# Optimization experiments

Measured on AMD Instinct MI355X. Metric: run time of the kernel, lower is better.

## Reference

```python
import jax, jax.numpy as jnp
import numpy as np

B, N, C = 64, 256, 512
SHIFTS = (-1, 0, 1)
# torch.chunk(N, 3): ceil(256/3)=86 -> sizes [86, 86, 84]
CHUNK_SIZES = (86, 86, 84)
EPS = 1e-5


def _shift_pad(a, s):
    # shift along last axis (C) with zero padding, matching shift_with_padding
    if s == 0:
        return a
    if s > 0:
        return jnp.pad(a[..., :-s], ((0, 0), (0, 0), (s, 0)))
    s = -s
    return jnp.pad(a[..., s:], ((0, 0), (0, 0), (0, s)))


def setup_inputs() -> dict:
    key = jax.random.key(0)
    ks = jax.random.split(key, 16)
    w = lambda k, shape: (jax.random.normal(k, shape, jnp.float32) * 0.02)
    inp = {
        "x": jax.random.normal(ks[0], (B, N, C), jnp.float32),
        "ln_g": jnp.ones((C,), jnp.float32),
        "ln_b": jnp.zeros((C,), jnp.float32),
        "Ws": w(ks[1], (C, C)),
        "bs": jnp.zeros((C,), jnp.float32),
        "Wc": w(ks[2], (N, N, 3)),     # Conv1d weight [out=N, in=N, k=3]
        "bc": jnp.zeros((N,), jnp.float32),
        "We1": w(ks[3], (N, N // 8)),
        "be1": jnp.zeros((N // 8,), jnp.float32),
        "We2": w(ks[4], (N // 8, N)),
        "be2": jnp.zeros((N,), jnp.float32),
        "Wf1": w(ks[5], (C, 2 * C)),
        "bf1": jnp.zeros((2 * C,), jnp.float32),
        "Wf2": w(ks[6], (2 * C, C)),
        "bf2": jnp.zeros((C,), jnp.float32),
    }
    return inp


def reference(x, ln_g, ln_b, Ws, bs, Wc, bc, We1, be1, We2, be2, Wf1, bf1, Wf2, bf2):
    res = x
    # channel_mixer_S: LayerNorm over C, then Linear C->C + relu (dropout=0)
    mu = jnp.mean(x, axis=-1, keepdims=True)
    var = jnp.mean((x - mu) ** 2, axis=-1, keepdims=True)
    h = (x - mu) * jax.lax.rsqrt(var + EPS) * ln_g + ln_b
    h = jax.nn.relu(h @ Ws + bs)                      # [B, N, C]
    # channel_shift: chunk along N, shift each chunk along C with zero pad
    offs = np.cumsum((0,) + CHUNK_SIZES)
    chunks = [h[:, offs[i]:offs[i + 1], :] for i in range(3)]
    x_shift = jnp.concatenate([_shift_pad(c, s) for c, s in zip(chunks, SHIFTS)], axis=1)
    # channel_projection: Conv1d over C with N channels, k=3, pad=1
    x_shift = jax.lax.conv_general_dilated(
        x_shift, Wc, window_strides=(1,), padding=[(1, 1)],
        dimension_numbers=("NCH", "OIH", "NCH")) + bc[None, :, None]
    # SE gating
    se = jnp.mean(x_shift, axis=-1)                   # [B, N]
    ex = jax.nn.sigmoid(jax.nn.relu(se @ We1 + be1) @ We2 + be2)  # [B, N]
    z = x_shift * ex[:, :, None]
    # channel_mixer_F: C -> 2C (relu) -> C, residual
    z = jax.nn.relu(z @ Wf1 + bf1) @ Wf2 + bf2 + res
    return z
```

## Files before the change

kernel.cpp:

```cpp
#include <hip/hip_runtime.h>
#include <hip/hip_bf16.h>
#include <math.h>

#define BB 64
#define NN 256
#define CCH 512

typedef unsigned short u16;
typedef __attribute__((ext_vector_type(8))) short s16x8;
typedef __attribute__((ext_vector_type(4))) float f32x4;

#define AS1 __attribute__((address_space(1)))
#define AS3 __attribute__((address_space(3)))

static __device__ __forceinline__ u16 f2b(float f) {
    __hip_bfloat16 h = __float2bfloat16(f);
    union { __hip_bfloat16 h; u16 u; } x; x.h = h; return x.u;
}
static __device__ __forceinline__ void gll16(const void* g, void* l) {
    __builtin_amdgcn_global_load_lds((const AS1 unsigned int*)g,
                                     (AS3 unsigned int*)l, 16, 0, 0);
}
static __device__ __forceinline__ int shf(int ni) {
    return (ni < 86) ? -1 : (ni < 172 ? 0 : 1);
}

#define VM8  asm volatile("s_waitcnt vmcnt(8)" ::: "memory")
#define VM6  asm volatile("s_waitcnt vmcnt(6)" ::: "memory")
#define VM0  asm volatile("s_waitcnt vmcnt(0)" ::: "memory")
#define LGKM0 asm volatile("s_waitcnt lgkmcnt(0)" ::: "memory")
#define MEMB asm volatile("" ::: "memory")

static __device__ __forceinline__ void wtc_body(const float* __restrict__ W,
    u16* __restrict__ Wt, int K, int N, int bx, int by, float* t, bool perm)
{
    int n0 = bx * 32, k0 = by * 32;
    int tx = threadIdx.x & 31, ty = threadIdx.x >> 5;
    #pragma unroll
    for (int i = 0; i < 4; ++i)
        t[(ty + i * 8) * 33 + tx] = W[(size_t)(k0 + ty + i * 8) * N + n0 + tx];
    __syncthreads();
    int kl = k0 + tx;
    int kp = perm ? ((kl & ~63) | ((kl & 15) << 2) | ((kl >> 4) & 3)) : kl;
    #pragma unroll
    for (int i = 0; i < 4; ++i)
        Wt[(size_t)(n0 + ty + i * 8) * K + kp] = f2b(t[tx * 33 + ty + i * 8]);
}

__global__ __launch_bounds__(256) void prep_ln_kernel(
    const float* __restrict__ Ws,  u16* __restrict__ Wst,
    const float* __restrict__ Wf1, u16* __restrict__ Wf1t,
    const float* __restrict__ Wf2, u16* __restrict__ Wf2t,
    const float* __restrict__ Wc,  u16* __restrict__ Wc3,
    u16* __restrict__ Hts,
    const float* __restrict__ x, const float* __restrict__ g,
    const float* __restrict__ bta, u16* __restrict__ xnorm)
{
    __shared__ float t[32 * 33];
    int bid = blockIdx.x;
    if (bid < 256) {
        wtc_body(Ws, Wst, 512, 512, bid & 15, bid >> 4, t, false);
    } else if (bid < 768) {
        int idx = bid - 256;
        wtc_body(Wf1, Wf1t, 512, 1024, idx & 31, idx >> 5, t, true);
    } else if (bid < 1280) {
        int idx = bid - 768;
        wtc_body(Wf2, Wf2t, 1024, 512, idx & 15, idx >> 4, t, true);
    } else if (bid < 2048) {
        int idx = (bid - 1280) * 256 + threadIdx.x;
        int xloc = idx & 255;
        int o = (idx >> 8) & 255;
        int k = idx >> 16;
        int il = (xloc & ~63) | ((xloc & 63) >> 2) | ((xloc & 3) << 4);
        Wc3[idx] = f2b(Wc[((size_t)o * NN + il) * 3 + k]);
    } else if (bid < 2304) {
        int idx = (bid - 2048) * 256 + threadIdx.x;
        int b   = idx >> 10;
        int rem = idx & 1023;
        int rr  = rem >> 8;
        int r   = (rr & 1) + (rr >> 1) * 512;
        Hts[((size_t)b * 514 + r) * 256 + (rem & 255)] = 0;
    } else {
        const int l = threadIdx.x & 63;
        const int r = (bid - 2304) * 4 + (threadIdx.x >> 6);
        const float4* xr = (const float4*)(x + (size_t)r * CCH);
        float4 v1 = xr[l];
        float4 v2 = xr[l + 64];
        float s  = v1.x + v1.y + v1.z + v1.w + v2.x + v2.y + v2.z + v2.w;
        float ss = v1.x*v1.x + v1.y*v1.y + v1.z*v1.z + v1.w*v1.w
                 + v2.x*v2.x + v2.y*v2.y + v2.z*v2.z + v2.w*v2.w;
        #pragma unroll
        for (int o = 32; o > 0; o >>= 1) {
            s  += __shfl_xor(s, o);
            ss += __shfl_xor(ss, o);
        }
        float mu  = s * (1.0f / CCH);
        float var = ss * (1.0f / CCH) - mu * mu;
        float rs  = rsqrtf(var + 1e-5f);
        float4 g1 = ((const float4*)g)[l],   g2 = ((const float4*)g)[l + 64];
        float4 b1 = ((const float4*)bta)[l], b2 = ((const float4*)bta)[l + 64];
        ushort4 o1, o2;
        o1.x = f2b((v1.x - mu) * rs * g1.x + b1.x);
        o1.y = f2b((v1.y - mu) * rs * g1.y + b1.y);
        o1.z = f2b((v1.z - mu) * rs * g1.z + b1.z);
        o1.w = f2b((v1.w - mu) * rs * g1.w + b1.w);
        o2.x = f2b((v2.x - mu) * rs * g2.x + b2.x);
        o2.y = f2b((v2.y - mu) * rs * g2.y + b2.y);
        o2.z = f2b((v2.z - mu) * rs * g2.z + b2.z);
        o2.w = f2b((v2.w - mu) * rs * g2.w + b2.w);
        ushort4* orow = (ushort4*)(xnorm + (size_t)r * CCH);
        orow[l]      = o1;
        orow[l + 64] = o2;
    }
}

template<int MODE>
__global__ __launch_bounds__(512, 1) void gemm_pipe(
    const u16* __restrict__ A, const u16* __restrict__ Bt,
    const float* __restrict__ bias, const float* __restrict__ res,
    void* __restrict__ outv, u16* __restrict__ auxout,
    float* __restrict__ SEpart)
{
    constexpr int NK = (MODE == 2) ? 32 : (MODE == 3) ? 24 : 16;
    constexpr int SA = (MODE == 2) ? 1024 : 512;
    constexpr int SB = (MODE == 2) ? 1024 : 512;

    __shared__ u16 Asm[6 * 8192];
    __shared__ u16 Bsm[6 * 4096];

    const int tid = threadIdx.x;
    const int l   = tid & 63;
    const int w   = tid >> 6;
    const int nwg = gridDim.x;
    const int work = (blockIdx.x & 7) * (nwg >> 3) + (blockIdx.x >> 3);

    int row0, col0, bidx = 0;
    if (MODE == 0)      { row0 = (work >> 7) * 256; col0 = (work & 127) * 128; }
    else if (MODE == 2) { row0 = (work >> 2) * 256; col0 = (work & 3) * 128; }
    else                { row0 = 0; bidx = work >> 2; col0 = (work & 3) * 128; }

    const u16* Aab  = A + (size_t)row0 * SA;
    const u16* Bab  = Bt + (size_t)col0 * SB;
    const u16* HtsB = Bt + (size_t)bidx * 514 * 256;

    const int wm = (w >> 1) * 64;
    const int wn = (w & 1) * 64;
    const int fr = l & 15;
    const int q  = l >> 4;
    const int kofs = ((q ^ ((l >> 1) & 3)) * 8);

    const f32x4 zero = {0.0f, 0.0f, 0.0f, 0.0f};
    f32x4 acc[4][4];
    #pragma unroll
    for (int m = 0; m < 4; ++m)
        #pragma unroll
        for (int n = 0; n < 4; ++n) acc[m][n] = zero;

    const int kc0 = ((tid & 3) ^ ((tid >> 3) & 3)) * 8;
    const int srow = tid >> 2;

    auto stage = [&](int u, int slot) {
        u16* ald = Asm + slot * 8192 + w * 512;
        u16* bld = Bsm + slot * 4096 + w * 512;
        if (MODE == 3) {
            const int kseg = u >> 3, kb = (u & 7) * 32 + kc0;
            gll16(A + kseg * 65536 + srow * 256 + kb, ald);
            gll16(A + kseg * 65536 + (srow + 128) * 256 + kb, ald + 4096);
            gll16(HtsB + (size_t)(col0 + srow + kseg) * 256 + kb, bld);
        } else {
            const int kb = u * 32 + kc0;
            gll16(Aab + (size_t)srow * SA + kb, ald);
            gll16(Aab + (size_t)(srow + 128) * SA + kb, ald + 4096);
            gll16(Bab + (size_t)srow * SB + kb, bld);
        }
    };

    stage(0, 0); stage(1, 1); stage(2, 2); stage(3, 3);
    int sa = 0;
    constexpr int NV = NK / 2;
    for (int v = 0; v < NV; ++v) {
        if (v + 1 < NV) { VM6; } else { VM0; }
        __builtin_amdgcn_s_barrier();
        MEMB;
        const int sb = sa + 1;
        s16x8 b0[4], af0[4];
        #pragma unroll
        for (int n = 0; n < 4; ++n)
            b0[n] = *(const s16x8*)&Bsm[sa * 4096 + (wn + n * 16 + fr) * 32 + kofs];
        #pragma unroll
        for (int m = 0; m < 4; ++m)
            af0[m] = *(const s16x8*)&Asm[sa * 8192 + (wm + m * 16 + fr) * 32 + kofs];
        const int u2 = 2 * v + 4;
        if (u2 < NK) {
            int st = sa + 4; if (st >= 6) st -= 6;
            stage(u2, st);
            int st1 = st + 1; if (st1 >= 6) st1 -= 6;
            stage(u2 + 1, st1);
        }
        __builtin_amdgcn_s_setprio(1);
        #pragma unroll
        for (int m = 0; m < 4; ++m)
            #pragma unroll
            for (int n = 0; n < 4; ++n)
                acc[m][n] = __builtin_amdgcn_mfma_f32_16x16x32_bf16(af0[m], b0[n], acc[m][n], 0, 0, 0);
        __builtin_amdgcn_s_setprio(0);
        s16x8 b1[4], af1[4];
        #pragma unroll
        for (int n = 0; n < 4; ++n)
            b1[n] = *(const s16x8*)&Bsm[sb * 4096 + (wn + n * 16 + fr) * 32 + kofs];
        #pragma unroll
        for (int m = 0; m < 4; ++m)
            af1[m] = *(const s16x8*)&Asm[sb * 8192 + (wm + m * 16 + fr) * 32 + kofs];
        __builtin_amdgcn_s_setprio(1);
        #pragma unroll
        for (int m = 0; m < 4; ++m)
            #pragma unroll
            for (int n = 0; n < 4; ++n)
                acc[m][n] = __builtin_amdgcn_mfma_f32_16x16x32_bf16(af1[m], b1[n], acc[m][n], 0, 0, 0);
        __builtin_amdgcn_s_setprio(0);
        MEMB;
        sa += 2; if (sa >= 6) sa = 0;
    }

    if (MODE == 0) {
        const int gb = col0 + wn;
        const int b  = gb >> 8;
        const int gl = gb & 255;
        const int nib = gl + fr;
        u16* HtsW = auxout + (size_t)b * 514 * 256;
        const int px = gl + 4 * fr;
        const int s0 = shf(nib), s3 = shf(nib + 48);
        #pragma unroll
        for (int m = 0; m < 4; ++m) {
            #pragma unroll
            for (int j = 0; j < 4; ++j) {
                const int c = row0 + wm + m * 16 + q * 4 + j;
                const float bsv = bias[c];
                u16 vv[4];
                #pragma unroll
                for (int n = 0; n < 4; ++n)
                    vv[n] = f2b(fmaxf(acc[m][n][j] + bsv, 0.0f));
                if (s0 == s3) {
                    ushort4 v4 = {vv[0], vv[1], vv[2], vv[3]};
                    *(ushort4*)&HtsW[(size_t)(c + 1 + s0) * 256 + px] = v4;
                } else {
                    #pragma unroll
                    for (int n = 0; n < 4; ++n)
                        HtsW[(size_t)(c + 1 + shf(nib + n * 16)) * 256 + px + n] = vv[n];
                }
            }
        }
    } else if (MODE == 2) {
        #pragma unroll
        for (int m = 0; m < 4; ++m) {
            #pragma unroll
            for (int j = 0; j < 4; ++j) {
                const int row = row0 + wm + m * 16 + q * 4 + j;
                #pragma unroll
                for (int n = 0; n < 4; ++n) {
                    const int col = col0 + wn + n * 16 + fr;
                    ((float*)outv)[(size_t)row * 512 + col] =
                        acc[m][n][j] + bias[col] + res[(size_t)row * 512 + col];
                }
            }
        }
    } else {
        const int cb = col0 + wn;
        const int px = cb + 4 * fr;
        const int sslot = (col0 >> 7) * 2 + (wn >> 6);
        #pragma unroll
        for (int m = 0; m < 4; ++m) {
            #pragma unroll
            for (int j = 0; j < 4; ++j) {
                const int no = wm + m * 16 + q * 4 + j;
                const float bcv = bias[no];
                float p = 0.0f;
                u16 vv[4];
                #pragma unroll
                for (int n = 0; n < 4; ++n) {
                    float v = acc[m][n][j];
                    vv[n] = f2b(v + bcv);
                    p += v;
                }
                ushort4 v4 = {vv[0], vv[1], vv[2], vv[3]};
                *(ushort4*)&auxout[((size_t)bidx * NN + no) * CCH + px] = v4;
                p += __shfl_xor(p, 1);
                p += __shfl_xor(p, 2);
                p += __shfl_xor(p, 4);
                p += __shfl_xor(p, 8);
                if (fr == 0)
                    SEpart[sslot * 16384 + bidx * NN + no] = p;
            }
        }
    }
}

__global__ __launch_bounds__(512, 1) void gemm1_8ph(
    const u16* __restrict__ Yb, const u16* __restrict__ Wf1t,
    const float* __restrict__ bf1, u16* __restrict__ T,
    const float* __restrict__ SEpart, const float* __restrict__ bc,
    const float* __restrict__ We1, const float* __restrict__ be1,
    const float* __restrict__ We2, const float* __restrict__ be2)
{
    __shared__ u16 Ab[2][256 * 64];
    __shared__ u16 Bb[2][256 * 64];
    __shared__ float sse[256];
    __shared__ float e1f[32];
    __shared__ float exs[256];

    const int tid = threadIdx.x;
    const int l   = tid & 63;
    const int w   = tid >> 6;
    const int work = (blockIdx.x & 7) * 32 + (blockIdx.x >> 3);
    const int row0 = (work >> 2) * 256;
    const int col0 = (work & 3) * 256;

    const u16* Aab = Yb  + (size_t)row0 * 512;
    const u16* Bab = Wf1t + (size_t)col0 * 512;

    const int wm = (w >> 2) * 128;
    const int wn = (w & 3) * 64;
    const int fr = l & 15;
    const int q  = l >> 4;
    const int r7 = fr & 7;

    if (tid < 256) {
        int o = row0 + tid;
        float sum = 0.0f;
        #pragma unroll
        for (int i = 0; i < 8; ++i) sum += SEpart[i * 16384 + o];
        sse[tid] = sum * (1.0f / CCH) + bc[tid];
    }
    __syncthreads();
    if (tid < 32) {
        float a = be1[tid];
        #pragma unroll 8
        for (int i = 0; i < 256; ++i) a += sse[i] * We1[i * 32 + tid];
        e1f[tid] = fmaxf(a, 0.0f);
    }
    __syncthreads();
    if (tid < 256) {
        float a = be2[tid];
        #pragma unroll
        for (int j = 0; j < 32; ++j) a += e1f[j] * We2[j * 256 + tid];
        exs[tid] = 1.0f / (1.0f + expf(-a));
    }
    __syncthreads();

    const int strow = tid >> 3;
    const int sslot = tid & 7;
    const int gslot = sslot ^ (strow & 7);
    const size_t goff = (size_t)strow * 512 + gslot * 8;
    const int     loff = strow * 64 + sslot * 8;

    auto stageA = [&](int c, int kt, int j) {
        gll16(Aab + (size_t)(j * 64) * 512 + kt * 64 + goff,
              &Ab[c][j * 64 * 64 + loff]);
    };
    auto stageB = [&](int c, int kt, int j) {
        gll16(Bab + (size_t)(j * 64) * 512 + kt * 64 + goff,
              &Bb[c][j * 64 * 64 + loff]);
    };

    stageA(0, 0, 0); stageA(0, 0, 1); stageA(0, 0, 2); stageA(0, 0, 3);
    stageB(0, 0, 0); stageB(0, 0, 1); stageB(0, 0, 2); stageB(0, 0, 3);
    stageA(1, 1, 0); stageA(1, 1, 2);
    stageB(1, 1, 0); stageB(1, 1, 1); stageB(1, 1, 2); stageB(1, 1, 3);

    const f32x4 zero = {0.0f, 0.0f, 0.0f, 0.0f};
    f32x4 acc[8][4];
    #pragma unroll
    for (int m = 0; m < 8; ++m)
        #pragma unroll
        for (int n = 0; n < 4; ++n) acc[m][n] = zero;

    s16x8 afv[4][2], bfv[4][2];

#define LDA8(c, r, ks) (*(const s16x8*)&Ab[c][(r) * 64 + (((((ks) << 2) + q) ^ r7) << 3)])
#define LDB8(c, r, ks) (*(const s16x8*)&Bb[c][(r) * 64 + (((((ks) << 2) + q) ^ r7) << 3)])

    for (int t = 0; t < 8; ++t) {
        const int c = t & 1;
        if (t < 7) { stageA(c ^ 1, t + 1, 1); stageA(c ^ 1, t + 1, 3); VM8; }
        else       { VM0; }
        __builtin_amdgcn_s_barrier();
        MEMB;
        #pragma unroll
        for (int m = 0; m < 4; ++m) {
            afv[m][0] = LDA8(c, wm + m * 16 + fr, 0);
            afv[m][1] = LDA8(c, wm + m * 16 + fr, 1);
        }
        #pragma unroll
        for (int n = 0; n < 2; ++n) {
            bfv[n][0] = LDB8(c, wn + n * 16 + fr, 0);
            bfv[n][1] = LDB8(c, wn + n * 16 + fr, 1);
        }
        LGKM0;
        __builtin_amdgcn_s_setprio(1);
        #pragma unroll
        for (int m = 0; m < 4; ++m)
            #pragma unroll
            for (int n = 0; n < 2; ++n) {
                acc[m][n] = __builtin_amdgcn_mfma_f32_16x16x32_bf16(afv[m][0], bfv[n][0], acc[m][n], 0, 0, 0);
                acc[m][n] = __builtin_amdgcn_mfma_f32_16x16x32_bf16(afv[m][1], bfv[n][1], acc[m][n], 0, 0, 0);
            }
        __builtin_amdgcn_s_setprio(0);
        __builtin_amdgcn_s_barrier();
        if (t < 6) { stageA(c, t + 2, 0); stageA(c, t + 2, 2); }
        #pragma unroll
        for (int n = 2; n < 4; ++n) {
            bfv[n][0] = LDB8(c, wn + n * 16 + fr, 0);
            bfv[n][1] = LDB8(c, wn + n * 16 + fr, 1);
        }
        LGKM0;
        __builtin_amdgcn_s_setprio(1);
        #pragma unroll
        for (int m = 0; m < 4; ++m)
            #pragma unroll
            for (int n = 2; n < 4; ++n) {
                acc[m][n] = __builtin_amdgcn_mfma_f32_16x16x32_bf16(afv[m][0], bfv[n][0], acc[m][n], 0, 0, 0);
                acc[m][n] = __builtin_amdgcn_mfma_f32_16x16x32_bf16(afv[m][1], bfv[n][1], acc[m][n], 0, 0, 0);
            }
        __builtin_amdgcn_s_setprio(0);
        __builtin_amdgcn_s_barrier();
        if (t < 6) { stageB(c, t + 2, 0); stageB(c, t + 2, 1); }
        #pragma unroll
        for (int m = 0; m < 4; ++m) {
            afv[m][0] = LDA8(c, wm + 64 + m * 16 + fr, 0);
            afv[m][1] = LDA8(c, wm + 64 + m * 16 + fr, 1);
        }
        LGKM0;
        __builtin_amdgcn_s_setprio(1);
        #pragma unroll
        for (int m = 0; m < 4; ++m)
            #pragma unroll
            for (int n = 0; n < 2; ++n) {
                acc[4 + m][n] = __builtin_amdgcn_mfma_f32_16x16x32_bf16(afv[m][0], bfv[n][0], acc[4 + m][n], 0, 0, 0);
                acc[4 + m][n] = __builtin_amdgcn_mfma_f32_16x16x32_bf16(afv[m][1], bfv[n][1], acc[4 + m][n], 0, 0, 0);
            }
        __builtin_amdgcn_s_setprio(0);
        __builtin_amdgcn_s_barrier();
        if (t < 6) { stageB(c, t + 2, 2); stageB(c, t + 2, 3); }
        __builtin_amdgcn_s_setprio(1);
        #pragma unroll
        for (int m = 0; m < 4; ++m)
            #pragma unroll
            for (int n = 2; n < 4; ++n) {
                acc[4 + m][n] = __builtin_amdgcn_mfma_f32_16x16x32_bf16(afv[m][0], bfv[n][0], acc[4 + m][n], 0, 0, 0);
                acc[4 + m][n] = __builtin_amdgcn_mfma_f32_16x16x32_bf16(afv[m][1], bfv[n][1], acc[4 + m][n], 0, 0, 0);
            }
        __builtin_amdgcn_s_setprio(0);
        __builtin_amdgcn_s_barrier();
    }

    const int cgb = col0 + wn;
    float bval[4];
    #pragma unroll
    for (int n = 0; n < 4; ++n) bval[n] = bf1[cgb + n * 16 + fr];
    #pragma unroll
    for (int m = 0; m < 8; ++m) {
        #pragma unroll
        for (int j = 0; j < 4; ++j) {
            const int rl  = wm + m * 16 + q * 4 + j;
            const int row = row0 + rl;
            const float sc = exs[rl];
            u16 vv[4];
            #pragma unroll
            for (int n = 0; n < 4; ++n)
                vv[n] = f2b(fmaxf(acc[m][n][j] * sc + bval[n], 0.0f));
            ushort4 v4 = {vv[0], vv[1], vv[2], vv[3]};
            *(ushort4*)&T[(size_t)row * 1024 + cgb + 4 * fr] = v4;
        }
    }
#undef LDA8
#undef LDB8
}

extern "C" void kernel_launch(void* const* d_in, const int* in_sizes, int n_in,
                              void* d_out, int out_size, void* d_ws, size_t ws_size,
                              hipStream_t stream) {
    const float* x    = (const float*)d_in[0];
    const float* ln_g = (const float*)d_in[1];
    const float* ln_b = (const float*)d_in[2];
    const float* Ws   = (const float*)d_in[3];
    const float* bs   = (const float*)d_in[4];
    const float* Wc   = (const float*)d_in[5];
    const float* bc   = (const float*)d_in[6];
    const float* We1  = (const float*)d_in[7];
    const float* be1  = (const float*)d_in[8];
    const float* We2  = (const float*)d_in[9];
    const float* be2  = (const float*)d_in[10];
    const float* Wf1  = (const float*)d_in[11];
    const float* bf1  = (const float*)d_in[12];
    const float* Wf2  = (const float*)d_in[13];
    const float* bf2  = (const float*)d_in[14];
    float* out = (float*)d_out;
    char* w8   = (char*)d_ws;

    u16* XN  = (u16*)(w8);
    u16* Y   = XN;
    u16* Hts = (u16*)(w8 + (16u << 20));
    u16* T   = (u16*)(w8 + (16u << 20));
    char* tail = w8 + 50397184;
    float* SEpart = (float*)(tail);
    u16* Wst      = (u16*)(tail + 524288);
    u16* Wf1t     = (u16*)(tail + 1048576);
    u16* Wf2t     = (u16*)(tail + 2097152);
    u16* Wc3      = (u16*)(tail + 3145728);

    prep_ln_kernel<<<6400, 256, 0, stream>>>(Ws, Wst, Wf1, Wf1t, Wf2, Wf2t,
                                             Wc, Wc3, Hts, x, ln_g, ln_b, XN);
    gemm_pipe<0><<<256, 512, 0, stream>>>(Wst, XN, bs, nullptr,
                                          nullptr, Hts, nullptr);
    gemm_pipe<3><<<256, 512, 0, stream>>>(Wc3, Hts, bc, nullptr,
                                          nullptr, Y, SEpart);
    gemm1_8ph<<<256, 512, 0, stream>>>(Y, Wf1t, bf1, T, SEpart, bc,
                                       We1, be1, We2, be2);
    gemm_pipe<2><<<256, 512, 0, stream>>>(T, Wf2t, bf2, x,
                                          out, nullptr, nullptr);
}
```

Measured before the change: 114.4 us.

## Fuse all stages into one persistent megakernel with grid barriers

Replaces the five separate launches (prep/layernorm, three GEMMs, FFN GEMM) with one persistent kernel of 256 blocks. The stages are separated by atomic-counter grid barriers, and LDS is shared through one raw buffer. The SE excitation MLP now runs once in 64 blocks and is written to a global buffer, where before every GEMM1 tile recomputed it. The aim is to remove launch gaps and that redundant SE work. In exchange the prep work runs as 25 serial iterations per block with only half the threads distinct, the workspace aliasing is removed so memory use grows, and a memset launch is added. The barrier's spin timeout can silently break correctness.

```diff
diff --git a/kernel.cpp b/kernel.cpp
--- a/kernel.cpp
+++ b/kernel.cpp
@@ -31,11 +31,27 @@
 #define LGKM0 asm volatile("s_waitcnt lgkmcnt(0)" ::: "memory")
 #define MEMB asm volatile("" ::: "memory")
 
+static __device__ __forceinline__ void gbar(unsigned* bar, unsigned target)
+{
+    __syncthreads();
+    if (threadIdx.x == 0) {
+        __threadfence();
+        __hip_atomic_fetch_add(bar, 1u, __ATOMIC_ACQ_REL, __HIP_MEMORY_SCOPE_AGENT);
+        unsigned spins = 0;
+        while (__hip_atomic_load(bar, __ATOMIC_ACQUIRE, __HIP_MEMORY_SCOPE_AGENT) < target) {
+            __builtin_amdgcn_s_sleep(2);
+            if (++spins > 4000000u) break;
+        }
+        __threadfence();
+    }
+    __syncthreads();
+}
+
 static __device__ __forceinline__ void wtc_body(const float* __restrict__ W,
-    u16* __restrict__ Wt, int K, int N, int bx, int by, float* t, bool perm)
+    u16* __restrict__ Wt, int K, int N, int bx, int by, float* t, bool perm, int t2)
 {
     int n0 = bx * 32, k0 = by * 32;
-    int tx = threadIdx.x & 31, ty = threadIdx.x >> 5;
+    int tx = t2 & 31, ty = t2 >> 5;
     #pragma unroll
     for (int i = 0; i < 4; ++i)
         t[(ty + i * 8) * 33 + tx] = W[(size_t)(k0 + ty + i * 8) * N + n0 + tx];
@@ -47,92 +63,23 @@
         Wt[(size_t)(n0 + ty + i * 8) * K + kp] = f2b(t[tx * 33 + ty + i * 8]);
 }
 
-__global__ __launch_bounds__(256) void prep_ln_kernel(
-    const float* __restrict__ Ws,  u16* __restrict__ Wst,
-    const float* __restrict__ Wf1, u16* __restrict__ Wf1t,
-    const float* __restrict__ Wf2, u16* __restrict__ Wf2t,
-    const float* __restrict__ Wc,  u16* __restrict__ Wc3,
-    u16* __restrict__ Hts,
-    const float* __restrict__ x, const float* __restrict__ g,
-    const float* __restrict__ bta, u16* __restrict__ xnorm)
-{
-    __shared__ float t[32 * 33];
-    int bid = blockIdx.x;
-    if (bid < 256) {
-        wtc_body(Ws, Wst, 512, 512, bid & 15, bid >> 4, t, false);
-    } else if (bid < 768) {
-        int idx = bid - 256;
-        wtc_body(Wf1, Wf1t, 512, 1024, idx & 31, idx >> 5, t, true);
-    } else if (bid < 1280) {
-        int idx = bid - 768;
-        wtc_body(Wf2, Wf2t, 1024, 512, idx & 15, idx >> 4, t, true);
-    } else if (bid < 2048) {
-        int idx = (bid - 1280) * 256 + threadIdx.x;
-        int xloc = idx & 255;
-        int o = (idx >> 8) & 255;
-        int k = idx >> 16;
-        int il = (xloc & ~63) | ((xloc & 63) >> 2) | ((xloc & 3) << 4);
-        Wc3[idx] = f2b(Wc[((size_t)o * NN + il) * 3 + k]);
-    } else if (bid < 2304) {
-        int idx = (bid - 2048) * 256 + threadIdx.x;
-        int b   = idx >> 10;
-        int rem = idx & 1023;
-        int rr  = rem >> 8;
-        int r   = (rr & 1) + (rr >> 1) * 512;
-        Hts[((size_t)b * 514 + r) * 256 + (rem & 255)] = 0;
-    } else {
-        const int l = threadIdx.x & 63;
-        const int r = (bid - 2304) * 4 + (threadIdx.x >> 6);
-        const float4* xr = (const float4*)(x + (size_t)r * CCH);
-        float4 v1 = xr[l];
-        float4 v2 = xr[l + 64];
-        float s  = v1.x + v1.y + v1.z + v1.w + v2.x + v2.y + v2.z + v2.w;
-        float ss = v1.x*v1.x + v1.y*v1.y + v1.z*v1.z + v1.w*v1.w
-                 + v2.x*v2.x + v2.y*v2.y + v2.z*v2.z + v2.w*v2.w;
-        #pragma unroll
-        for (int o = 32; o > 0; o >>= 1) {
-            s  += __shfl_xor(s, o);
-            ss += __shfl_xor(ss, o);
-        }
-        float mu  = s * (1.0f / CCH);
-        float var = ss * (1.0f / CCH) - mu * mu;
-        float rs  = rsqrtf(var + 1e-5f);
-        float4 g1 = ((const float4*)g)[l],   g2 = ((const float4*)g)[l + 64];
-        float4 b1 = ((const float4*)bta)[l], b2 = ((const float4*)bta)[l + 64];
-        ushort4 o1, o2;
-        o1.x = f2b((v1.x - mu) * rs * g1.x + b1.x);
-        o1.y = f2b((v1.y - mu) * rs * g1.y + b1.y);
-        o1.z = f2b((v1.z - mu) * rs * g1.z + b1.z);
-        o1.w = f2b((v1.w - mu) * rs * g1.w + b1.w);
-        o2.x = f2b((v2.x - mu) * rs * g2.x + b2.x);
-        o2.y = f2b((v2.y - mu) * rs * g2.y + b2.y);
-        o2.z = f2b((v2.z - mu) * rs * g2.z + b2.z);
-        o2.w = f2b((v2.w - mu) * rs * g2.w + b2.w);
-        ushort4* orow = (ushort4*)(xnorm + (size_t)r * CCH);
-        orow[l]      = o1;
-        orow[l + 64] = o2;
-    }
-}
-
 template<int MODE>
-__global__ __launch_bounds__(512, 1) void gemm_pipe(
+static __device__ void gemm_phase(
     const u16* __restrict__ A, const u16* __restrict__ Bt,
     const float* __restrict__ bias, const float* __restrict__ res,
     void* __restrict__ outv, u16* __restrict__ auxout,
-    float* __restrict__ SEpart)
+    float* __restrict__ SEpart, char* ldsraw, const int bid, const int tid)
 {
     constexpr int NK = (MODE == 2) ? 32 : (MODE == 3) ? 24 : 16;
     constexpr int SA = (MODE == 2) ? 1024 : 512;
     constexpr int SB = (MODE == 2) ? 1024 : 512;
 
-    __shared__ u16 Asm[6 * 8192];
-    __shared__ u16 Bsm[6 * 4096];
-
-    const int tid = threadIdx.x;
-    const int l   = tid & 63;
-    const int w   = tid >> 6;
-    const int nwg = gridDim.x;
-    const int work = (blockIdx.x & 7) * (nwg >> 3) + (blockIdx.x >> 3);
+    u16* Asm = (u16*)ldsraw;
+    u16* Bsm = (u16*)(ldsraw + 98304);
+
+    const int l = tid & 63;
+    const int w = tid >> 6;
+    const int work = (bid & 7) * 32 + (bid >> 3);
 
     int row0, col0, bidx = 0;
     if (MODE == 0)      { row0 = (work >> 7) * 256; col0 = (work & 127) * 128; }
@@ -295,27 +242,22 @@
     }
 }
 
-__global__ __launch_bounds__(512, 1) void gemm1_8ph(
+static __device__ void gemm1_phase(
     const u16* __restrict__ Yb, const u16* __restrict__ Wf1t,
     const float* __restrict__ bf1, u16* __restrict__ T,
-    const float* __restrict__ SEpart, const float* __restrict__ bc,
-    const float* __restrict__ We1, const float* __restrict__ be1,
-    const float* __restrict__ We2, const float* __restrict__ be2)
+    const float* __restrict__ EX, char* ldsraw, const int bid, const int tid)
 {
-    __shared__ u16 Ab[2][256 * 64];
-    __shared__ u16 Bb[2][256 * 64];
-    __shared__ float sse[256];
-    __shared__ float e1f[32];
-    __shared__ float exs[256];
-
-    const int tid = threadIdx.x;
-    const int l   = tid & 63;
-    const int w   = tid >> 6;
-    const int work = (blockIdx.x & 7) * 32 + (blockIdx.x >> 3);
+    u16* Ab0 = (u16*)ldsraw;
+    u16* Bb0 = (u16*)(ldsraw + 65536);
+    float* exs = (float*)(ldsraw + 131072);
+
+    const int l = tid & 63;
+    const int w = tid >> 6;
+    const int work = (bid & 7) * 32 + (bid >> 3);
     const int row0 = (work >> 2) * 256;
     const int col0 = (work & 3) * 256;
 
-    const u16* Aab = Yb  + (size_t)row0 * 512;
+    const u16* Aab = Yb   + (size_t)row0 * 512;
     const u16* Bab = Wf1t + (size_t)col0 * 512;
 
     const int wm = (w >> 2) * 128;
@@ -324,27 +266,7 @@
     const int q  = l >> 4;
     const int r7 = fr & 7;
 
-    if (tid < 256) {
-        int o = row0 + tid;
-        float sum = 0.0f;
-        #pragma unroll
-        for (int i = 0; i < 8; ++i) sum += SEpart[i * 16384 + o];
-        sse[tid] = sum * (1.0f / CCH) + bc[tid];
-    }
-    __syncthreads();
-    if (tid < 32) {
-        float a = be1[tid];
-        #pragma unroll 8
-        for (int i = 0; i < 256; ++i) a += sse[i] * We1[i * 32 + tid];
-        e1f[tid] = fmaxf(a, 0.0f);
-    }
-    __syncthreads();
-    if (tid < 256) {
-        float a = be2[tid];
-        #pragma unroll
-        for (int j = 0; j < 32; ++j) a += e1f[j] * We2[j * 256 + tid];
-        exs[tid] = 1.0f / (1.0f + expf(-a));
-    }
+    if (tid < 256) exs[tid] = EX[row0 + tid];
     __syncthreads();
 
     const int strow = tid >> 3;
@@ -355,11 +277,11 @@
 
     auto stageA = [&](int c, int kt, int j) {
         gll16(Aab + (size_t)(j * 64) * 512 + kt * 64 + goff,
-              &Ab[c][j * 64 * 64 + loff]);
+              &Ab0[c * 16384 + j * 64 * 64 + loff]);
     };
     auto stageB = [&](int c, int kt, int j) {
         gll16(Bab + (size_t)(j * 64) * 512 + kt * 64 + goff,
-              &Bb[c][j * 64 * 64 + loff]);
+              &Bb0[c * 16384 + j * 64 * 64 + loff]);
     };
 
     stageA(0, 0, 0); stageA(0, 0, 1); stageA(0, 0, 2); stageA(0, 0, 3);
@@ -376,8 +298,8 @@
 
     s16x8 afv[4][2], bfv[4][2];
 
-#define LDA8(c, r, ks) (*(const s16x8*)&Ab[c][(r) * 64 + (((((ks) << 2) + q) ^ r7) << 3)])
-#define LDB8(c, r, ks) (*(const s16x8*)&Bb[c][(r) * 64 + (((((ks) << 2) + q) ^ r7) << 3)])
+#define LDA8(c, r, ks) (*(const s16x8*)&Ab0[(c) * 16384 + (r) * 64 + (((((ks) << 2) + q) ^ r7) << 3)])
+#define LDB8(c, r, ks) (*(const s16x8*)&Bb0[(c) * 16384 + (r) * 64 + (((((ks) << 2) + q) ^ r7) << 3)])
 
     for (int t = 0; t < 8; ++t) {
         const int c = t & 1;
@@ -474,6 +396,127 @@
     }
 #undef LDA8
 #undef LDB8
+}
+
+__global__ __launch_bounds__(512, 1) void mega_kernel(
+    const float* __restrict__ x, const float* __restrict__ ln_g,
+    const float* __restrict__ ln_b,
+    const float* __restrict__ Ws,  const float* __restrict__ bs,
+    const float* __restrict__ Wc,  const float* __restrict__ bc,
+    const float* __restrict__ We1, const float* __restrict__ be1,
+    const float* __restrict__ We2, const float* __restrict__ be2,
+    const float* __restrict__ Wf1, const float* __restrict__ bf1,
+    const float* __restrict__ Wf2, const float* __restrict__ bf2,
+    float* __restrict__ out,
+    u16* XN, u16* Y, u16* Hts, u16* T,
+    u16* Wst, u16* Wf1t, u16* Wf2t, u16* Wc3,
+    float* SEpart, float* EX, unsigned* bar)
+{
+    __shared__ __align__(16) char ldsraw[147456];
+    const int tid = threadIdx.x;
+    const int bid = blockIdx.x;
+
+    {
+        float* t = (float*)ldsraw;
+        for (int it = 0; it < 25; ++it) {
+            const int ob = bid * 25 + it;
+            __syncthreads();
+            const int t2 = tid & 255;
+            if (ob < 256) {
+                wtc_body(Ws, Wst, 512, 512, ob & 15, ob >> 4, t, false, t2);
+            } else if (ob < 768) {
+                int idx = ob - 256;
+                wtc_body(Wf1, Wf1t, 512, 1024, idx & 31, idx >> 5, t, true, t2);
+            } else if (ob < 1280) {
+                int idx = ob - 768;
+                wtc_body(Wf2, Wf2t, 1024, 512, idx & 15, idx >> 4, t, true, t2);
+            } else if (ob < 2048) {
+                int idx = (ob - 1280) * 256 + t2;
+                int xloc = idx & 255;
+                int o = (idx >> 8) & 255;
+                int k = idx >> 16;
+                int il = (xloc & ~63) | ((xloc & 63) >> 2) | ((xloc & 3) << 4);
+                Wc3[idx] = f2b(Wc[((size_t)o * NN + il) * 3 + k]);
+            } else if (ob < 2304) {
+                int idx = (ob - 2048) * 256 + t2;
+                int b   = idx >> 10;
+                int rem = idx & 1023;
+                int rr  = rem >> 8;
+                int r   = (rr & 1) + (rr >> 1) * 512;
+                Hts[((size_t)b * 514 + r) * 256 + (rem & 255)] = 0;
+            } else {
+                const int l = t2 & 63;
+                const int r = (ob - 2304) * 4 + (t2 >> 6);
+                const float4* xr = (const float4*)(x + (size_t)r * CCH);
+                float4 v1 = xr[l];
+                float4 v2 = xr[l + 64];
+                float s  = v1.x + v1.y + v1.z + v1.w + v2.x + v2.y + v2.z + v2.w;
+                float ss = v1.x*v1.x + v1.y*v1.y + v1.z*v1.z + v1.w*v1.w
+                         + v2.x*v2.x + v2.y*v2.y + v2.z*v2.z + v2.w*v2.w;
+                #pragma unroll
+                for (int o = 32; o > 0; o >>= 1) {
+                    s  += __shfl_xor(s, o);
+                    ss += __shfl_xor(ss, o);
+                }
+                float mu  = s * (1.0f / CCH);
+                float var = ss * (1.0f / CCH) - mu * mu;
+                float rs  = rsqrtf(var + 1e-5f);
+                float4 g1 = ((const float4*)ln_g)[l],   g2 = ((const float4*)ln_g)[l + 64];
+                float4 b1 = ((const float4*)ln_b)[l],   b2 = ((const float4*)ln_b)[l + 64];
+                ushort4 o1, o2;
+                o1.x = f2b((v1.x - mu) * rs * g1.x + b1.x);
+                o1.y = f2b((v1.y - mu) * rs * g1.y + b1.y);
+                o1.z = f2b((v1.z - mu) * rs * g1.z + b1.z);
+                o1.w = f2b((v1.w - mu) * rs * g1.w + b1.w);
+                o2.x = f2b((v2.x - mu) * rs * g2.x + b2.x);
+                o2.y = f2b((v2.y - mu) * rs * g2.y + b2.y);
+                o2.z = f2b((v2.z - mu) * rs * g2.z + b2.z);
+                o2.w = f2b((v2.w - mu) * rs * g2.w + b2.w);
+                ushort4* orow = (ushort4*)(XN + (size_t)r * CCH);
+                orow[l]      = o1;
+                orow[l + 64] = o2;
+            }
+        }
+    }
+    gbar(bar, 256);
+
+    gemm_phase<0>(Wst, XN, bs, nullptr, nullptr, Hts, nullptr, ldsraw, bid, tid);
+    gbar(bar, 512);
+
+    gemm_phase<3>(Wc3, Hts, bc, nullptr, nullptr, Y, SEpart, ldsraw, bid, tid);
+    gbar(bar, 768);
+
+    if (bid < 64) {
+        float* sse = (float*)ldsraw;
+        float* e1f = (float*)(ldsraw + 1024);
+        if (tid < 256) {
+            int o = bid * 256 + tid;
+            float sum = 0.0f;
+            #pragma unroll
+            for (int i = 0; i < 8; ++i) sum += SEpart[i * 16384 + o];
+            sse[tid] = sum * (1.0f / CCH) + bc[tid];
+        }
+        __syncthreads();
+        if (tid < 32) {
+            float a = be1[tid];
+            #pragma unroll 8
+            for (int i = 0; i < 256; ++i) a += sse[i] * We1[i * 32 + tid];
+            e1f[tid] = fmaxf(a, 0.0f);
+        }
+        __syncthreads();
+        if (tid < 256) {
+            float a = be2[tid];
+            #pragma unroll
+            for (int j = 0; j < 32; ++j) a += e1f[j] * We2[j * 256 + tid];
+            EX[bid * 256 + tid] = 1.0f / (1.0f + expf(-a));
+        }
+    }
+    gbar(bar, 1024);
+
+    gemm1_phase(Y, Wf1t, bf1, T, EX, ldsraw, bid, tid);
+    gbar(bar, 1280);
+
+    gemm_phase<2>(T, Wf2t, bf2, x, out, nullptr, nullptr, ldsraw, bid, tid);
 }
 
 extern "C" void kernel_launch(void* const* d_in, const int* in_sizes, int n_in,
@@ -498,24 +541,21 @@
     char* w8   = (char*)d_ws;
 
     u16* XN  = (u16*)(w8);
-    u16* Y   = XN;
-    u16* Hts = (u16*)(w8 + (16u << 20));
-    u16* T   = (u16*)(w8 + (16u << 20));
-    char* tail = w8 + 50397184;
+    u16* Y   = (u16*)(w8 + 16777216);
+    u16* Hts = (u16*)(w8 + 33554432);
+    u16* T   = (u16*)(w8 + 50397184);
+    char* tail = w8 + 83951616;
     float* SEpart = (float*)(tail);
     u16* Wst      = (u16*)(tail + 524288);
     u16* Wf1t     = (u16*)(tail + 1048576);
     u16* Wf2t     = (u16*)(tail + 2097152);
     u16* Wc3      = (u16*)(tail + 3145728);
-
-    prep_ln_kernel<<<6400, 256, 0, stream>>>(Ws, Wst, Wf1, Wf1t, Wf2, Wf2t,
-                                             Wc, Wc3, Hts, x, ln_g, ln_b, XN);
-    gemm_pipe<0><<<256, 512, 0, stream>>>(Wst, XN, bs, nullptr,
-                                          nullptr, Hts, nullptr);
-    gemm_pipe<3><<<256, 512, 0, stream>>>(Wc3, Hts, bc, nullptr,
-                                          nullptr, Y, SEpart);
-    gemm1_8ph<<<256, 512, 0, stream>>>(Y, Wf1t, bf1, T, SEpart, bc,
-                                       We1, be1, We2, be2);
-    gemm_pipe<2><<<256, 512, 0, stream>>>(T, Wf2t, bf2, x,
-                                          out, nullptr, nullptr);
-}
+    float* EX     = (float*)(tail + 3538944);
+    unsigned* bar = (unsigned*)(tail + 3604480);
+
+    hipMemsetAsync(bar, 0, 64, stream);
+    mega_kernel<<<256, 512, 0, stream>>>(
+        x, ln_g, ln_b, Ws, bs, Wc, bc, We1, be1, We2, be2,
+        Wf1, bf1, Wf2, bf2, out,
+        XN, Y, Hts, T, Wst, Wf1t, Wf2t, Wc3, SEpart, EX, bar);
+}
```

New measurement: 293.3 us. +156.3%, slower.
